# Kernel tuning notes

Hardware: AMD Instinct MI355X
Metric: run time of the kernel (lower is better)

Reference implementation:

```python
import jax, jax.numpy as jnp
import numpy as np

NUM_BINS = 15
THRESHOLD = 0.01


def setup_inputs() -> dict:
    key = jax.random.key(0)
    k1, k2 = jax.random.split(key)
    N, C = 500000, 100
    probas = jax.random.uniform(k1, (N, C), dtype=jnp.float32)
    labels = jax.random.randint(k2, (N,), 0, C, dtype=jnp.int64)
    return {"probas": probas, "labels": labels}


def reference(probas, labels):
    # probas: [N, C] float, labels: [N] int
    N, C = probas.shape
    B = NUM_BINS
    bins = jnp.linspace(0.0, 1.0, B + 1, dtype=probas.dtype)  # [B+1]

    # bin index: bins[lo] <= p < bins[lo+1] (side='right' => right edge strict)
    lo = jnp.searchsorted(bins, probas, side='right') - 1      # [N, C]
    lo_c = jnp.clip(lo, 0, B - 1)
    left_edge = bins[lo_c]
    # original uses strict inequalities on BOTH edges, plus threshold filter
    valid = (probas > THRESHOLD) & (lo >= 0) & (lo < B) & (probas > left_edge)
    w = valid.astype(probas.dtype)                              # [N, C]

    # segment id = class * B + bin, flattened over [N, C]
    cols = jnp.broadcast_to(jnp.arange(C), (N, C))
    seg = (cols * B + lo_c).ravel()
    num_seg = C * B

    correct = (labels[:, None] == jnp.arange(C)[None, :]).astype(probas.dtype)

    count = jax.ops.segment_sum(w.ravel(), seg, num_segments=num_seg)
    sum_p = jax.ops.segment_sum((probas * w).ravel(), seg, num_segments=num_seg)
    sum_a = jax.ops.segment_sum((correct * w).ravel(), seg, num_segments=num_seg)

    nan = jnp.asarray(jnp.nan, probas.dtype)
    denom = jnp.maximum(count, 1.0)
    confs = jnp.where(count > 0, sum_p / denom, nan).reshape(C, B)
    accs = jnp.where(count > 0, sum_a / denom, nan).reshape(C, B)
    n_samples = count.reshape(C, B)
    return confs, accs, n_samples
```

## Files before the change

kernel.cpp:

```cpp
#include <hip/hip_runtime.h>

#define NBINS 15
#define NCLS  100
#define NSEG  (NBINS * NCLS)
#define NGRP  64
#define NBLK  512
#define BLK   1024
#define SUMSCALE 2048.0f
#define INV15 (1.0f / 15.0f)

typedef float nf4 __attribute__((ext_vector_type(4)));

__device__ __forceinline__ void proc_f4(nf4 v, int i,
                                        const int* __restrict__ labels,
                                        unsigned int* s_pk, unsigned int* s_ac)
{
    int row  = i / 25;
    int col0 = (i - row * 25) * 4;
    int lbl  = labels[row];
    float pv[4] = {v.x, v.y, v.z, v.w};
    #pragma unroll
    for (int j = 0; j < 4; ++j) {
        float p = pv[j];
        int c = col0 + j;
        int k = (int)(p * 15.0f);
        if (k < NBINS && (float)(k + 1) * INV15 <= p)      ++k;
        else if (k > 0 && (float)k * INV15 > p)            --k;
        float left = (float)k * INV15;
        if (p > 0.01f && k < NBINS && p > left) {
            int seg = c * NBINS + k;
            unsigned int pk = (1u << 20) | (unsigned int)(p * SUMSCALE + 0.5f);
            atomicAdd(&s_pk[seg], pk);
            if (lbl == c) atomicAdd(&s_ac[seg], 1u);
        }
    }
}

__global__ __launch_bounds__(BLK) void calib_accum(
    const float* __restrict__ probas,
    const int*   __restrict__ labels,
    unsigned int* __restrict__ partU,
    int total4)
{
    __shared__ unsigned int s_pk[NSEG];
    __shared__ unsigned int s_ac[NSEG];
    const int t = threadIdx.x;
    for (int i = t; i < NSEG; i += BLK) { s_pk[i] = 0u; s_ac[i] = 0u; }
    __syncthreads();

    const nf4* __restrict__ p4 = (const nf4*)probas;
    const int stride = gridDim.x * BLK;
    const int half4  = total4 >> 1;

    for (int i = blockIdx.x * BLK + t; i < half4; i += stride) {
        nf4 a = __builtin_nontemporal_load(&p4[i]);
        nf4 b = __builtin_nontemporal_load(&p4[i + half4]);
        proc_f4(a, i,         labels, s_pk, s_ac);
        proc_f4(b, i + half4, labels, s_pk, s_ac);
    }
    if ((total4 & 1) && blockIdx.x == 0 && t == 0) {
        proc_f4(p4[total4 - 1], total4 - 1, labels, s_pk, s_ac);
    }
    __syncthreads();

    unsigned int* dst = partU + (size_t)blockIdx.x * (2 * NSEG);
    for (int s = t; s < NSEG; s += BLK) {
        dst[s]        = s_pk[s];
        dst[NSEG + s] = s_ac[s];
    }
}

__global__ __launch_bounds__(256) void calib_mid(
    const unsigned int* __restrict__ partU, int nblk, int chunk,
    unsigned int*       __restrict__ partB)
{
    int t = blockIdx.x * 256 + threadIdx.x;
    if (t >= NGRP * NSEG) return;
    int g = t / NSEG;
    int s = t - g * NSEG;
    int b0 = g * chunk;
    int b1 = b0 + chunk; if (b1 > nblk) b1 = nblk;
    unsigned int cnt = 0u, sumq = 0u, acc = 0u;
    for (int b = b0; b < b1; ++b) {
        const unsigned int* src = partU + (size_t)b * (2 * NSEG);
        unsigned int pk = src[s];
        cnt  += pk >> 20;
        sumq += pk & 0xFFFFFu;
        acc  += src[NSEG + s];
    }
    unsigned int* dst = partB + (size_t)g * (3 * NSEG);
    dst[s]            = cnt;
    dst[NSEG + s]     = sumq;
    dst[2 * NSEG + s] = acc;
}

__global__ __launch_bounds__(256) void calib_fin(
    const unsigned int* __restrict__ partB,
    float*              __restrict__ out)
{
    int s = blockIdx.x * 256 + threadIdx.x;
    if (s >= NSEG) return;
    unsigned int cnt = 0u, sumq = 0u, acc = 0u;
    #pragma unroll
    for (int g = 0; g < NGRP; ++g) {
        const unsigned int* src = partB + g * (3 * NSEG);
        cnt  += src[s];
        sumq += src[NSEG + s];
        acc  += src[2 * NSEG + s];
    }
    float conf, accv;
    if (cnt > 0u) {
        float inv = 1.0f / (float)cnt;
        conf = (float)sumq * (1.0f / SUMSCALE) * inv;
        accv = (float)acc * inv;
    } else {
        conf = __int_as_float(0x7fc00000);
        accv = conf;
    }
    out[s]            = conf;
    out[NSEG + s]     = accv;
    out[2 * NSEG + s] = (float)cnt;
}

extern "C" void kernel_launch(void* const* d_in, const int* in_sizes, int n_in,
                              void* d_out, int out_size, void* d_ws, size_t ws_size,
                              hipStream_t stream) {
    const float* probas = (const float*)d_in[0];
    const int*   labels = (const int*)d_in[1];
    float* out = (float*)d_out;
    unsigned int* ws = (unsigned int*)d_ws;

    int total  = in_sizes[0];
    int total4 = total / 4;

    size_t ws_u32 = ws_size / sizeof(unsigned int);
    long long avail = (long long)ws_u32 - (long long)NGRP * 3 * NSEG;
    int nblk = (int)(avail / (2 * NSEG));
    if (nblk > NBLK) nblk = NBLK;
    if (nblk < 1) nblk = 1;

    unsigned int* partU = ws;
    unsigned int* partB = ws + (size_t)nblk * (2 * NSEG);

    calib_accum<<<nblk, BLK, 0, stream>>>(probas, labels, partU, total4);
    int chunk = (nblk + NGRP - 1) / NGRP;
    calib_mid<<<(NGRP * NSEG + 255) / 256, 256, 0, stream>>>(partU, nblk, chunk, partB);
    calib_fin<<<(NSEG + 255) / 256, 256, 0, stream>>>(partB, out);
}
```

Baseline: 280.8 us.

## Merge two-stage partial reduction into single block-reduced finalize kernel

Replaces the mid-level reduction kernel and the final kernel with one finalize kernel. Each block handles 32 segments with 8 thread groups, each summing a chunk of per-block partials, then combines them in shared memory and writes the outputs. This removes one kernel launch and the intermediate partB buffer round trip. In exchange the finalize kernel runs with only 47 blocks, so there is less parallelism for reading the 512 partials.

Result: no change. 282.9 us (+0.7%).

```diff
diff --git a/kernel.cpp b/kernel.cpp
--- a/kernel.cpp
+++ b/kernel.cpp
@@ -3,9 +3,9 @@
 #define NBINS 15
 #define NCLS  100
 #define NSEG  (NBINS * NCLS)
-#define NGRP  64
 #define NBLK  512
 #define BLK   1024
+#define FBLK  256
 #define SUMSCALE 2048.0f
 #define INV15 (1.0f / 15.0f)
 
@@ -70,56 +70,55 @@
     }
 }
 
-__global__ __launch_bounds__(256) void calib_mid(
-    const unsigned int* __restrict__ partU, int nblk, int chunk,
-    unsigned int*       __restrict__ partB)
-{
-    int t = blockIdx.x * 256 + threadIdx.x;
-    if (t >= NGRP * NSEG) return;
-    int g = t / NSEG;
-    int s = t - g * NSEG;
-    int b0 = g * chunk;
-    int b1 = b0 + chunk; if (b1 > nblk) b1 = nblk;
-    unsigned int cnt = 0u, sumq = 0u, acc = 0u;
-    for (int b = b0; b < b1; ++b) {
-        const unsigned int* src = partU + (size_t)b * (2 * NSEG);
-        unsigned int pk = src[s];
-        cnt  += pk >> 20;
-        sumq += pk & 0xFFFFFu;
-        acc  += src[NSEG + s];
-    }
-    unsigned int* dst = partB + (size_t)g * (3 * NSEG);
-    dst[s]            = cnt;
-    dst[NSEG + s]     = sumq;
-    dst[2 * NSEG + s] = acc;
-}
-
-__global__ __launch_bounds__(256) void calib_fin(
-    const unsigned int* __restrict__ partB,
+__global__ __launch_bounds__(FBLK) void calib_fin2(
+    const unsigned int* __restrict__ partU, int nblk,
     float*              __restrict__ out)
 {
-    int s = blockIdx.x * 256 + threadIdx.x;
-    if (s >= NSEG) return;
+    __shared__ unsigned int s_cnt[FBLK], s_sum[FBLK], s_acc[FBLK];
+    const int t   = threadIdx.x;
+    const int ts  = t & 31;
+    const int tb  = t >> 5;
+    const int seg = blockIdx.x * 32 + ts;
+    const int chunk = (nblk + 7) >> 3;
+    int b0 = tb * chunk;
+    int b1 = b0 + chunk; if (b1 > nblk) b1 = nblk;
+
     unsigned int cnt = 0u, sumq = 0u, acc = 0u;
+    if (seg < NSEG) {
+        for (int b = b0; b < b1; ++b) {
+            const unsigned int* src = partU + (size_t)b * (2 * NSEG);
+            unsigned int pk = src[seg];
+            cnt  += pk >> 20;
+            sumq += pk & 0xFFFFFu;
+            acc  += src[NSEG + seg];
+        }
+    }
+    s_cnt[t] = cnt; s_sum[t] = sumq; s_acc[t] = acc;
+    __syncthreads();
     #pragma unroll
-    for (int g = 0; g < NGRP; ++g) {
-        const unsigned int* src = partB + g * (3 * NSEG);
-        cnt  += src[s];
-        sumq += src[NSEG + s];
-        acc  += src[2 * NSEG + s];
+    for (int off = 4; off >= 1; off >>= 1) {
+        if (tb < off) {
+            s_cnt[t] += s_cnt[t + off * 32];
+            s_sum[t] += s_sum[t + off * 32];
+            s_acc[t] += s_acc[t + off * 32];
+        }
+        __syncthreads();
     }
-    float conf, accv;
-    if (cnt > 0u) {
-        float inv = 1.0f / (float)cnt;
-        conf = (float)sumq * (1.0f / SUMSCALE) * inv;
-        accv = (float)acc * inv;
-    } else {
-        conf = __int_as_float(0x7fc00000);
-        accv = conf;
+    if (tb == 0 && seg < NSEG) {
+        unsigned int c = s_cnt[t], sq = s_sum[t], a = s_acc[t];
+        float conf, accv;
+        if (c > 0u) {
+            float inv = 1.0f / (float)c;
+            conf = (float)sq * (1.0f / SUMSCALE) * inv;
+            accv = (float)a * inv;
+        } else {
+            conf = __int_as_float(0x7fc00000);
+            accv = conf;
+        }
+        out[seg]            = conf;
+        out[NSEG + seg]     = accv;
+        out[2 * NSEG + seg] = (float)c;
     }
-    out[s]            = conf;
-    out[NSEG + s]     = accv;
-    out[2 * NSEG + s] = (float)cnt;
 }
 
 extern "C" void kernel_launch(void* const* d_in, const int* in_sizes, int n_in,
@@ -134,16 +133,12 @@
     int total4 = total / 4;
 
     size_t ws_u32 = ws_size / sizeof(unsigned int);
-    long long avail = (long long)ws_u32 - (long long)NGRP * 3 * NSEG;
-    int nblk = (int)(avail / (2 * NSEG));
+    int nblk = (int)(ws_u32 / (2 * NSEG));
     if (nblk > NBLK) nblk = NBLK;
     if (nblk < 1) nblk = 1;
 
     unsigned int* partU = ws;
-    unsigned int* partB = ws + (size_t)nblk * (2 * NSEG);
 
     calib_accum<<<nblk, BLK, 0, stream>>>(probas, labels, partU, total4);
-    int chunk = (nblk + NGRP - 1) / NGRP;
-    calib_mid<<<(NGRP * NSEG + 255) / 256, 256, 0, stream>>>(partU, nblk, chunk, partB);
-    calib_fin<<<(NSEG + 255) / 256, 256, 0, stream>>>(partB, out);
+    calib_fin2<<<(NSEG + 31) / 32, FBLK, 0, stream>>>(partU, nblk, out);
 }
```
